# Optimization experiments

Hardware: AMD Instinct MI355X
Metric: run time of the kernel (lower is better)

Reference implementation:

```python
import jax, jax.numpy as jnp
import numpy as np


def setup_inputs() -> dict:
    key = jax.random.key(0)
    k1, k2 = jax.random.split(key)
    B, T, D = 8, 2048, 2048
    layer_in = jax.random.normal(k1, (B, T, D), dtype=jnp.float32)
    # nn.Linear(2D, 2D): weight [out=2D, in=2D], bias [2D]
    W_gate = jax.random.normal(k2, (2 * D, 2 * D), dtype=jnp.float32) * 0.02
    b_gate = jnp.zeros((2 * D,), dtype=jnp.float32)
    return {"layer_in": layer_in, "W_gate": W_gate, "b_gate": b_gate}


def reference(layer_in, W_gate, b_gate):
    # Cumulative average: tril(ones)/row_index @ x  ==  cumsum(x)/[1..t]
    t = layer_in.shape[1]
    denom = jnp.arange(1, t + 1, dtype=layer_in.dtype)[:, None]  # (t, 1)
    average_out = jnp.cumsum(layer_in, axis=1) / denom  # (B, t, D)
    # Gating: Linear(2D -> 2D) on concat(x, avg), then chunk into two gates
    gating_in = jnp.concatenate([layer_in, average_out], axis=-1)  # (B, t, 2D)
    gates = jnp.einsum('btk,ok->bto', gating_in, W_gate) + b_gate  # (B, t, 2D)
    input_gate, forget_gate = jnp.split(gates, 2, axis=2)
    gating_out = (jax.nn.sigmoid(input_gate) * layer_in
                  + jax.nn.sigmoid(forget_gate) * average_out)
    return gating_out, average_out
```

## Files before the change

### kernel.cpp

```cpp
#include <hip/hip_runtime.h>
#include <hip/hip_bf16.h>


#define Bb 8
#define Tt 2048
#define Dd 2048
#define Mm (Bb * Tt)
#define Kk 4096
#define NC 32
#define CT 64

typedef __bf16 bf16x8 __attribute__((ext_vector_type(8)));
typedef float f32x4 __attribute__((ext_vector_type(4)));

__device__ __forceinline__ void gload16(const void* g, void* l) {
    __builtin_amdgcn_global_load_lds(
        (const __attribute__((address_space(1))) unsigned int*)g,
        (__attribute__((address_space(3))) unsigned int*)l, 16, 0, 0);
}

__global__ void wconv_kernel(const float* __restrict__ W,
                             unsigned short* __restrict__ Wb, long n) {
    long i = ((long)blockIdx.x * blockDim.x + threadIdx.x) * 4;
    long stride = (long)gridDim.x * blockDim.x * 4;
    for (; i < n; i += stride) {
        float4 v = *(const float4*)(W + i);
        __hip_bfloat16 a = __float2bfloat16(v.x);
        __hip_bfloat16 b = __float2bfloat16(v.y);
        __hip_bfloat16 c = __float2bfloat16(v.z);
        __hip_bfloat16 d = __float2bfloat16(v.w);
        ushort4 u;
        u.x = *(unsigned short*)&a; u.y = *(unsigned short*)&b;
        u.z = *(unsigned short*)&c; u.w = *(unsigned short*)&d;
        *(ushort4*)(Wb + i) = u;
    }
}

__global__ void ksum_kernel(const float* __restrict__ X, float* __restrict__ S,
                            unsigned short* __restrict__ Gin) {
    int d = blockIdx.y * 256 + threadIdx.x;
    int bc = blockIdx.x;
    int b = bc >> 5, c = bc & 31;
    const float* p = X + ((long)(b * Tt + c * CT)) * Dd + d;
    long row = (long)b * Tt + c * CT;
    float s = 0.f;
#pragma unroll 8
    for (int t = 0; t < CT; ++t) {
        float x = p[(long)t * Dd];
        s += x;
        __hip_bfloat16 xb = __float2bfloat16(x);
        Gin[(row + t) * 4096 + d] = *(unsigned short*)&xb;
    }
    S[(long)bc * Dd + d] = s;
}

__global__ void kscan_kernel(const unsigned short* __restrict__ Ginx,
                             const float* __restrict__ S,
                             float* __restrict__ AVG, unsigned short* __restrict__ Gin) {
    int d = blockIdx.y * 256 + threadIdx.x;
    int bc = blockIdx.x;
    int b = bc >> 5, c = bc & 31;
    const float* Sp = S + (long)(b * NC) * Dd + d;
    float run = 0.f;
    for (int cc = 0; cc < c; ++cc) run += Sp[(long)cc * Dd];
    long row = (long)b * Tt + c * CT;
    for (int tt = 0; tt < CT; ++tt) {
        long r = row + tt;
        union { unsigned int u; float f; } cx;
        cx.u = ((unsigned int)Ginx[r * 4096 + d]) << 16;
        run += cx.f;
        float av = run / (float)(c * CT + tt + 1);
        AVG[r * Dd + d] = av;
        __hip_bfloat16 ab = __float2bfloat16(av);
        Gin[r * 4096 + 2048 + d] = *(unsigned short*)&ab;
    }
}

#define MFMA(va, vb, c_) c_ = __builtin_amdgcn_mfma_f32_16x16x32_bf16(va, vb, c_, 0, 0, 0)
#define RD(p_, i_) (*(const bf16x8*)((p_) + (i_) * 1024))
#define SBAR __builtin_amdgcn_s_barrier()
#define SCHB __builtin_amdgcn_sched_barrier(0)
#define LGKM0 do { asm volatile("s_waitcnt lgkmcnt(0)" ::: "memory"); SCHB; } while (0)

#define CL_LO(B0_, B1_, B2_, B3_)                                               \
    __builtin_amdgcn_s_setprio(1);                                              \
    MFMA(aL0,B0_,acc[0][0]); MFMA(aL0,B1_,acc[0][1]); MFMA(aL0,B2_,acc[0][2]); MFMA(aL0,B3_,acc[0][3]); \
    MFMA(aL1,B0_,acc[1][0]); MFMA(aL1,B1_,acc[1][1]); MFMA(aL1,B2_,acc[1][2]); MFMA(aL1,B3_,acc[1][3]); \
    MFMA(aL2,B0_,acc[2][0]); MFMA(aL2,B1_,acc[2][1]); MFMA(aL2,B2_,acc[2][2]); MFMA(aL2,B3_,acc[2][3]); \
    MFMA(aL3,B0_,acc[3][0]); MFMA(aL3,B1_,acc[3][1]); MFMA(aL3,B2_,acc[3][2]); MFMA(aL3,B3_,acc[3][3]); \
    __builtin_amdgcn_s_setprio(0);
#define CL_HI(B0_, B1_, B2_, B3_)                                               \
    __builtin_amdgcn_s_setprio(1);                                              \
    MFMA(aH0,B0_,acc[4][0]); MFMA(aH0,B1_,acc[4][1]); MFMA(aH0,B2_,acc[4][2]); MFMA(aH0,B3_,acc[4][3]); \
    MFMA(aH1,B0_,acc[5][0]); MFMA(aH1,B1_,acc[5][1]); MFMA(aH1,B2_,acc[5][2]); MFMA(aH1,B3_,acc[5][3]); \
    MFMA(aH2,B0_,acc[6][0]); MFMA(aH2,B1_,acc[6][1]); MFMA(aH2,B2_,acc[6][2]); MFMA(aH2,B3_,acc[6][3]); \
    MFMA(aH3,B0_,acc[7][0]); MFMA(aH3,B1_,acc[7][1]); MFMA(aH3,B2_,acc[7][2]); MFMA(aH3,B3_,acc[7][3]); \
    __builtin_amdgcn_s_setprio(0);

#define TILE64(t_, bb_, STG_, VM_, VB_)                                         \
  {                                                                             \
    const char* pa_ = rA0 + (bb_);                                              \
    const char* pb_ = rB0 + (bb_);                                              \
    char* nb_ = ldsb + ((bb_) ^ 65536) + woff;                                  \
    const long ko_ = ((long)(t_) + 1) * 128;                                    \
                         \
    aL0 = RD(pa_,0); aL1 = RD(pa_,1); aL2 = RD(pa_,2); aL3 = RD(pa_,3);         \
    bb0 = RD(pb_,0); bb1 = RD(pb_,1); bb2 = RD(pb_,2); bb3 = RD(pb_,3);         \
    if (STG_) { gload16(gA0 + ko_, nb_); gload16(gA1 + ko_, nb_ + 8192); }      \
    LGKM0;                                                         \
                                      \
    aH0 = RD(pa_,4); aH1 = RD(pa_,5); aH2 = RD(pa_,6); aH3 = RD(pa_,7);         \
    SCHB;                                                                       \
    CL_LO(bb0, bb1, bb2, bb3)                                                   \
    SCHB;                                                                       \
    asm volatile("s_waitcnt vmcnt(" #VM_ ")" ::: "memory");                     \
    SBAR; SCHB;                                             \
    LGKM0;                                                         \
             \
    aL0 = RD(pa_+32768,0); aL1 = RD(pa_+32768,1); aL2 = RD(pa_+32768,2); aL3 = RD(pa_+32768,3); \
    bd0 = RD(pb_+32768,0); bd1 = RD(pb_+32768,1); bd2 = RD(pb_+32768,2); bd3 = RD(pb_+32768,3); \
    if (STG_) { gload16(gB0 + ko_, nb_ + 16384); gload16(gB1 + ko_, nb_ + 24576); } \
    SCHB;                                                                       \
    CL_HI(bb0, bb1, bb2, bb3)                                                   \
    SCHB;                                                                       \
    LGKM0;                                                         \
                     \
    aH0 = RD(pa_+32768,4); aH1 = RD(pa_+32768,5); aH2 = RD(pa_+32768,6); aH3 = RD(pa_+32768,7); \
    if (STG_) { gload16(gA0 + ko_ + 64, nb_ + 32768); gload16(gA1 + ko_ + 64, nb_ + 40960); } \
    SCHB;                                                                       \
    CL_LO(bd0, bd1, bd2, bd3)                                                   \
    SCHB;                                                                       \
    LGKM0;                                                         \
                                         \
    if (STG_) { gload16(gB0 + ko_ + 64, nb_ + 49152); gload16(gB1 + ko_ + 64, nb_ + 57344); } \
    SCHB;                                                                       \
    CL_HI(bd0, bd1, bd2, bd3)                                                   \
    SCHB;                                                                       \
    asm volatile("s_waitcnt vmcnt(" #VB_ ")" ::: "memory");                     \
    SBAR; SCHB;                                           \
  }

__global__ __launch_bounds__(512, 1) void gemmsp_kernel(
    const unsigned short* __restrict__ Gin,
    const unsigned short* __restrict__ Wb,
    const float* __restrict__ bias,
    float* __restrict__ OUT)
{
    __shared__ __attribute__((aligned(128))) char lds[131072];
    char* ldsb = (char*)lds;

    const int tid = threadIdx.x;
    const int w = tid >> 6, l = tid & 63;
    const int wm = w >> 2, wn = w & 3;
    const int lm = l & 15;
    const int woff = w * 1024;

    const int bid = blockIdx.x;
    const int batch = bid >> 8;
    const int rr = bid & 255;
    const int xcd = rr & 7;
    const int j = rr >> 3;
    const int nt = xcd * 2 + (j >> 4);
    const int mt = batch * 16 + (j & 15);
    const long m0 = (long)mt * 256;
    const int n0 = nt * 128;

    const int srow = tid >> 2;
    const int schunk = (tid & 3) ^ ((tid >> 3) & 3);
    const char* gA0 = (const char*)Gin + (m0 + srow) * 8192 + schunk * 16;
    const char* gA1 = gA0 + 128 * 8192;
    const long jr0 = n0 + ((srow >> 6) << 5) + (srow & 31) + (((srow >> 5) & 1) << 11);
    const int j1 = 128 + srow;
    const long jr1 = n0 + ((j1 >> 6) << 5) + (j1 & 31) + (((j1 >> 5) & 1) << 11);
    const char* gB0 = (const char*)Wb + jr0 * 8192 + schunk * 16;
    const char* gB1 = (const char*)Wb + jr1 * 8192 + schunk * 16;

    const int cbyte = (((l >> 4) ^ ((lm >> 1) & 3))) * 16;
    const char* rA0 = ldsb + (wm * 128 + lm) * 64 + cbyte;
    const char* rB0 = ldsb + 16384 + (wn * 64 + lm) * 64 + cbyte;

    f32x4 acc[8][4] = {};

    bf16x8 aL0, aL1, aL2, aL3, aH0, aH1, aH2, aH3;
    bf16x8 bb0, bb1, bb2, bb3, bd0, bd1, bd2, bd3;

    gload16(gA0,      ldsb + woff);
    gload16(gA1,      ldsb + 8192 + woff);
    gload16(gB0,      ldsb + 16384 + woff);
    gload16(gB1,      ldsb + 24576 + woff);
    gload16(gA0 + 64, ldsb + 32768 + woff);
    gload16(gA1 + 64, ldsb + 40960 + woff);
    gload16(gB0 + 64, ldsb + 49152 + woff);
    gload16(gB1 + 64, ldsb + 57344 + woff);
    asm volatile("s_waitcnt vmcnt(4)" ::: "memory");
    SBAR; SCHB;

#pragma unroll 1
    for (int t = 0; t < 62; t += 2) {
        TILE64(t,     0,     1, 2, 4)
        TILE64(t + 1, 65536, 1, 2, 4)
    }
    TILE64(62, 0,     1, 2, 4)
    TILE64(63, 65536, 0, 0, 0)

#pragma unroll
    for (int mi = 0; mi < 8; ++mi) {
        long rbase = m0 + wm * 128 + mi * 16 + (l >> 4) * 4;
#pragma unroll
        for (int nj = 0; nj < 2; ++nj) {
            int d = n0 + wn * 32 + nj * 16 + lm;
            float bi_ = bias[d];
            float bf_ = bias[d + 2048];
#pragma unroll
            for (int r = 0; r < 4; ++r) {
                long row = rbase + r;
                unsigned int ux = Gin[row * 4096 + d];
                unsigned int ua = Gin[row * 4096 + 2048 + d];
                union { unsigned int u; float f; } cx, ca;
                cx.u = ux << 16; ca.u = ua << 16;
                float gi = acc[mi][nj][r] + bi_;
                float gf = acc[mi][nj + 2][r] + bf_;
                float si = 1.f / (1.f + __expf(-gi));
                float sf = 1.f / (1.f + __expf(-gf));
                OUT[row * 2048 + d] = si * cx.f + sf * ca.f;
            }
        }
    }
}

extern "C" void kernel_launch(void* const* d_in, const int* in_sizes, int n_in,
                              void* d_out, int out_size, void* d_ws, size_t ws_size,
                              hipStream_t stream) {
    const float* X = (const float*)d_in[0];
    const float* W = (const float*)d_in[1];
    const float* bias = (const float*)d_in[2];

    float* OUT = (float*)d_out;
    float* AVG = OUT + (long)Mm * Dd;

    char* ws = (char*)d_ws;
    unsigned short* Wb  = (unsigned short*)ws;
    unsigned short* Gin = (unsigned short*)(ws + 33554432);
    float* S = (float*)(ws + 33554432 + 134217728);

    wconv_kernel<<<2048, 256, 0, stream>>>(W, Wb, (long)Kk * Kk);
    ksum_kernel<<<dim3(Bb * NC, Dd / 256), 256, 0, stream>>>(X, S, Gin);
    kscan_kernel<<<dim3(Bb * NC, Dd / 256), 256, 0, stream>>>(Gin, S, AVG, Gin);
    gemmsp_kernel<<<1024, 512, 0, stream>>>(Gin, Wb, bias, OUT);
}
```

Before: 597.4 us.

## Switch GEMM to 32x32x16 MFMA with k-major unswizzled LDS layout

Replaces the 16x16x32 bf16 MFMA tiling with 32x32x16 MFMAs, so each wave computes a 128x64 output using 4x2 accumulators of 16 floats. The LDS staging layout changes from swizzled rows to a k-chunk-major layout, and the global-to-LDS address mapping and fragment reads change to match. The goal is fewer MFMA issues and fewer LDS reads per FLOP. The risks are LDS bank conflicts from dropping the XOR swizzle and different register pressure. The epilogue is remapped to the 32x32 accumulator row layout.

```diff
diff --git a/kernel.cpp b/kernel.cpp
--- a/kernel.cpp
+++ b/kernel.cpp
@@ -11,7 +11,7 @@
 #define CT 64
 
 typedef __bf16 bf16x8 __attribute__((ext_vector_type(8)));
-typedef float f32x4 __attribute__((ext_vector_type(4)));
+typedef float f32x16 __attribute__((ext_vector_type(16)));
 
 __device__ __forceinline__ void gload16(const void* g, void* l) {
     __builtin_amdgcn_global_load_lds(
@@ -76,71 +76,67 @@
     }
 }
 
-#define MFMA(va, vb, c_) c_ = __builtin_amdgcn_mfma_f32_16x16x32_bf16(va, vb, c_, 0, 0, 0)
-#define RD(p_, i_) (*(const bf16x8*)((p_) + (i_) * 1024))
+#define MFMA32(va, vb, c_) c_ = __builtin_amdgcn_mfma_f32_32x32x16_bf16(va, vb, c_, 0, 0, 0)
 #define SBAR __builtin_amdgcn_s_barrier()
 #define SCHB __builtin_amdgcn_sched_barrier(0)
 #define LGKM0 do { asm volatile("s_waitcnt lgkmcnt(0)" ::: "memory"); SCHB; } while (0)
 
-#define CL_LO(B0_, B1_, B2_, B3_)                                               \
+#define READ6(S_, off_)                                                         \
+    S_##a0 = *(const bf16x8*)(rAc + (off_));                                    \
+    S_##a1 = *(const bf16x8*)(rAc + (off_) + 512);                              \
+    S_##a2 = *(const bf16x8*)(rAc + (off_) + 1024);                             \
+    S_##a3 = *(const bf16x8*)(rAc + (off_) + 1536);                             \
+    S_##b0 = *(const bf16x8*)(rBc + (off_));                                    \
+    S_##b1 = *(const bf16x8*)(rBc + (off_) + 8192);
+
+#define CLUST(S_)                                                               \
     __builtin_amdgcn_s_setprio(1);                                              \
-    MFMA(aL0,B0_,acc[0][0]); MFMA(aL0,B1_,acc[0][1]); MFMA(aL0,B2_,acc[0][2]); MFMA(aL0,B3_,acc[0][3]); \
-    MFMA(aL1,B0_,acc[1][0]); MFMA(aL1,B1_,acc[1][1]); MFMA(aL1,B2_,acc[1][2]); MFMA(aL1,B3_,acc[1][3]); \
-    MFMA(aL2,B0_,acc[2][0]); MFMA(aL2,B1_,acc[2][1]); MFMA(aL2,B2_,acc[2][2]); MFMA(aL2,B3_,acc[2][3]); \
-    MFMA(aL3,B0_,acc[3][0]); MFMA(aL3,B1_,acc[3][1]); MFMA(aL3,B2_,acc[3][2]); MFMA(aL3,B3_,acc[3][3]); \
+    MFMA32(S_##a0, S_##b0, acc[0][0]); MFMA32(S_##a0, S_##b1, acc[0][1]);       \
+    MFMA32(S_##a1, S_##b0, acc[1][0]); MFMA32(S_##a1, S_##b1, acc[1][1]);       \
+    MFMA32(S_##a2, S_##b0, acc[2][0]); MFMA32(S_##a2, S_##b1, acc[2][1]);       \
+    MFMA32(S_##a3, S_##b0, acc[3][0]); MFMA32(S_##a3, S_##b1, acc[3][1]);       \
     __builtin_amdgcn_s_setprio(0);
-#define CL_HI(B0_, B1_, B2_, B3_)                                               \
-    __builtin_amdgcn_s_setprio(1);                                              \
-    MFMA(aH0,B0_,acc[4][0]); MFMA(aH0,B1_,acc[4][1]); MFMA(aH0,B2_,acc[4][2]); MFMA(aH0,B3_,acc[4][3]); \
-    MFMA(aH1,B0_,acc[5][0]); MFMA(aH1,B1_,acc[5][1]); MFMA(aH1,B2_,acc[5][2]); MFMA(aH1,B3_,acc[5][3]); \
-    MFMA(aH2,B0_,acc[6][0]); MFMA(aH2,B1_,acc[6][1]); MFMA(aH2,B2_,acc[6][2]); MFMA(aH2,B3_,acc[6][3]); \
-    MFMA(aH3,B0_,acc[7][0]); MFMA(aH3,B1_,acc[7][1]); MFMA(aH3,B2_,acc[7][2]); MFMA(aH3,B3_,acc[7][3]); \
-    __builtin_amdgcn_s_setprio(0);
-
-#define TILE64(t_, bb_, STG_, VM_, VB_)                                         \
+
+#define TILE32R(t_, bb_, STG_, VM_, VB_)                                        \
   {                                                                             \
-    const char* pa_ = rA0 + (bb_);                                              \
-    const char* pb_ = rB0 + (bb_);                                              \
     char* nb_ = ldsb + ((bb_) ^ 65536) + woff;                                  \
     const long ko_ = ((long)(t_) + 1) * 128;                                    \
-                         \
-    aL0 = RD(pa_,0); aL1 = RD(pa_,1); aL2 = RD(pa_,2); aL3 = RD(pa_,3);         \
-    bb0 = RD(pb_,0); bb1 = RD(pb_,1); bb2 = RD(pb_,2); bb3 = RD(pb_,3);         \
+                                  \
+    READ6(p, (bb_))                                                             \
     if (STG_) { gload16(gA0 + ko_, nb_); gload16(gA1 + ko_, nb_ + 8192); }      \
-    LGKM0;                                                         \
-                                      \
-    aH0 = RD(pa_,4); aH1 = RD(pa_,5); aH2 = RD(pa_,6); aH3 = RD(pa_,7);         \
-    SCHB;                                                                       \
-    CL_LO(bb0, bb1, bb2, bb3)                                                   \
+    LGKM0;                                                        \
+                    \
+    READ6(q, (bb_) + 4096)                                                      \
+    SCHB;                                                                       \
+    CLUST(p)                                                                    \
     SCHB;                                                                       \
     asm volatile("s_waitcnt vmcnt(" #VM_ ")" ::: "memory");                     \
     SBAR; SCHB;                                             \
-    LGKM0;                                                         \
-             \
-    aL0 = RD(pa_+32768,0); aL1 = RD(pa_+32768,1); aL2 = RD(pa_+32768,2); aL3 = RD(pa_+32768,3); \
-    bd0 = RD(pb_+32768,0); bd1 = RD(pb_+32768,1); bd2 = RD(pb_+32768,2); bd3 = RD(pb_+32768,3); \
+    LGKM0;                                                        \
+                \
+    READ6(p, (bb_) + 32768)                                                     \
     if (STG_) { gload16(gB0 + ko_, nb_ + 16384); gload16(gB1 + ko_, nb_ + 24576); } \
     SCHB;                                                                       \
-    CL_HI(bb0, bb1, bb2, bb3)                                                   \
-    SCHB;                                                                       \
-    LGKM0;                                                         \
-                     \
-    aH0 = RD(pa_+32768,4); aH1 = RD(pa_+32768,5); aH2 = RD(pa_+32768,6); aH3 = RD(pa_+32768,7); \
+    CLUST(q)                                                                    \
+    SCHB;                                                                       \
+    LGKM0;                                                        \
+                      \
+    READ6(q, (bb_) + 36864)                                                     \
     if (STG_) { gload16(gA0 + ko_ + 64, nb_ + 32768); gload16(gA1 + ko_ + 64, nb_ + 40960); } \
     SCHB;                                                                       \
-    CL_LO(bd0, bd1, bd2, bd3)                                                   \
-    SCHB;                                                                       \
-    LGKM0;                                                         \
-                                         \
+    CLUST(p)                                                                    \
+    SCHB;                                                                       \
+    LGKM0;                                                        \
+                               \
     if (STG_) { gload16(gB0 + ko_ + 64, nb_ + 49152); gload16(gB1 + ko_ + 64, nb_ + 57344); } \
     SCHB;                                                                       \
-    CL_HI(bd0, bd1, bd2, bd3)                                                   \
+    CLUST(q)                                                                    \
     SCHB;                                                                       \
     asm volatile("s_waitcnt vmcnt(" #VB_ ")" ::: "memory");                     \
     SBAR; SCHB;                                           \
   }
 
-__global__ __launch_bounds__(512, 1) void gemmsp_kernel(
+__global__ __launch_bounds__(512, 1) void gemm32r2_kernel(
     const unsigned short* __restrict__ Gin,
     const unsigned short* __restrict__ Wb,
     const float* __restrict__ bias,
@@ -152,7 +148,8 @@
     const int tid = threadIdx.x;
     const int w = tid >> 6, l = tid & 63;
     const int wm = w >> 2, wn = w & 3;
-    const int lm = l & 15;
+    const int la = l & 31;
+    const int lk = l >> 5;
     const int woff = w * 1024;
 
     const int bid = blockIdx.x;
@@ -165,24 +162,20 @@
     const long m0 = (long)mt * 256;
     const int n0 = nt * 128;
 
-    const int srow = tid >> 2;
-    const int schunk = (tid & 3) ^ ((tid >> 3) & 3);
-    const char* gA0 = (const char*)Gin + (m0 + srow) * 8192 + schunk * 16;
+    const int r128 = tid & 127;
+    const int ch = tid >> 7;
+    const char* gA0 = (const char*)Gin + (m0 + r128) * 8192 + ch * 16;
     const char* gA1 = gA0 + 128 * 8192;
-    const long jr0 = n0 + ((srow >> 6) << 5) + (srow & 31) + (((srow >> 5) & 1) << 11);
-    const int j1 = 128 + srow;
-    const long jr1 = n0 + ((j1 >> 6) << 5) + (j1 & 31) + (((j1 >> 5) & 1) << 11);
-    const char* gB0 = (const char*)Wb + jr0 * 8192 + schunk * 16;
-    const char* gB1 = (const char*)Wb + jr1 * 8192 + schunk * 16;
-
-    const int cbyte = (((l >> 4) ^ ((lm >> 1) & 3))) * 16;
-    const char* rA0 = ldsb + (wm * 128 + lm) * 64 + cbyte;
-    const char* rB0 = ldsb + 16384 + (wn * 64 + lm) * 64 + cbyte;
-
-    f32x4 acc[8][4] = {};
-
-    bf16x8 aL0, aL1, aL2, aL3, aH0, aH1, aH2, aH3;
-    bf16x8 bb0, bb1, bb2, bb3, bd0, bd1, bd2, bd3;
+    const char* gB0 = (const char*)Wb + ((long)(n0 + r128)) * 8192 + ch * 16;
+    const char* gB1 = (const char*)Wb + ((long)(2048 + n0 + r128)) * 8192 + ch * 16;
+
+    const char* rAc = ldsb + wm * 8192 + lk * 2048 + la * 16;
+    const char* rBc = ldsb + 16384 + lk * 2048 + (wn * 32 + la) * 16;
+
+    f32x16 acc[4][2] = {};
+
+    bf16x8 pa0, pa1, pa2, pa3, pb0, pb1;
+    bf16x8 qa0, qa1, qa2, qa3, qb0, qb1;
 
     gload16(gA0,      ldsb + woff);
     gload16(gA1,      ldsb + 8192 + woff);
@@ -197,33 +190,32 @@
 
 #pragma unroll 1
     for (int t = 0; t < 62; t += 2) {
-        TILE64(t,     0,     1, 2, 4)
-        TILE64(t + 1, 65536, 1, 2, 4)
-    }
-    TILE64(62, 0,     1, 2, 4)
-    TILE64(63, 65536, 0, 0, 0)
-
+        TILE32R(t,     0,     1, 2, 4)
+        TILE32R(t + 1, 65536, 1, 2, 4)
+    }
+    TILE32R(62, 0,     1, 2, 4)
+    TILE32R(63, 65536, 0, 0, 0)
+
+    const int d = n0 + wn * 32 + la;
+    const float bi_ = bias[d];
+    const float bf_ = bias[d + 2048];
 #pragma unroll
-    for (int mi = 0; mi < 8; ++mi) {
-        long rbase = m0 + wm * 128 + mi * 16 + (l >> 4) * 4;
+    for (int mi = 0; mi < 4; ++mi) {
+        const long rb = m0 + wm * 128 + mi * 32 + lk * 4;
+        f32x16 ci = acc[mi][0];
+        f32x16 cf = acc[mi][1];
 #pragma unroll
-        for (int nj = 0; nj < 2; ++nj) {
-            int d = n0 + wn * 32 + nj * 16 + lm;
-            float bi_ = bias[d];
-            float bf_ = bias[d + 2048];
-#pragma unroll
-            for (int r = 0; r < 4; ++r) {
-                long row = rbase + r;
-                unsigned int ux = Gin[row * 4096 + d];
-                unsigned int ua = Gin[row * 4096 + 2048 + d];
-                union { unsigned int u; float f; } cx, ca;
-                cx.u = ux << 16; ca.u = ua << 16;
-                float gi = acc[mi][nj][r] + bi_;
-                float gf = acc[mi][nj + 2][r] + bf_;
-                float si = 1.f / (1.f + __expf(-gi));
-                float sf = 1.f / (1.f + __expf(-gf));
-                OUT[row * 2048 + d] = si * cx.f + sf * ca.f;
-            }
+        for (int qq = 0; qq < 16; ++qq) {
+            long row = rb + (qq & 3) + 8 * (qq >> 2);
+            unsigned int ux = Gin[row * 4096 + d];
+            unsigned int ua = Gin[row * 4096 + 2048 + d];
+            union { unsigned int u; float f; } cx, ca;
+            cx.u = ux << 16; ca.u = ua << 16;
+            float gi = ci[qq] + bi_;
+            float gf = cf[qq] + bf_;
+            float si = 1.f / (1.f + __expf(-gi));
+            float sf = 1.f / (1.f + __expf(-gf));
+            OUT[row * 2048 + d] = si * cx.f + sf * ca.f;
         }
     }
 }
@@ -246,5 +238,5 @@
     wconv_kernel<<<2048, 256, 0, stream>>>(W, Wb, (long)Kk * Kk);
     ksum_kernel<<<dim3(Bb * NC, Dd / 256), 256, 0, stream>>>(X, S, Gin);
     kscan_kernel<<<dim3(Bb * NC, Dd / 256), 256, 0, stream>>>(Gin, S, AVG, Gin);
-    gemmsp_kernel<<<1024, 512, 0, stream>>>(Gin, Wb, bias, OUT);
-}
+    gemm32r2_kernel<<<1024, 512, 0, stream>>>(Gin, Wb, bias, OUT);
+}
```

Measured after the change: 786.8 us. 1.32x slower.
